# Performance work log

Measured on AMD Instinct MI355X. Metric: run time of the kernel, lower is better.

Reference implementation:

```python
import jax, jax.numpy as jnp
import numpy as np

B, T, S, H, D = 4, 2048, 2048, 16, 64


def setup_inputs() -> dict:
    key = jax.random.key(0)
    kq, kkv = jax.random.split(key)
    q = jax.random.normal(kq, (B, T, H, D), dtype=jnp.float32)
    kv = jax.random.normal(kkv, (B, S, 2, H, D), dtype=jnp.float32)
    return {"q": q, "kv": kv}


def reference(q, kv):
    # q: [B,T,H,D]; kv: [B,S,2,H,D] (packed k and v)
    k = kv[:, :, 0]  # [B,S,H,D]
    v = kv[:, :, 1]  # [B,S,H,D]
    scale = 1.0 / jnp.sqrt(jnp.asarray(q.shape[-1], q.dtype))
    # scores: [B,H,T,S]
    scores = jnp.einsum("bthd,bshd->bhts", q, k) * scale
    probs = jax.nn.softmax(scores, axis=-1)
    out = jnp.einsum("bhts,bshd->bthd", probs, v)  # [B,T,H,D]
    return out
```

## Files before the change

kernel.cpp:

```cpp
#include <hip/hip_runtime.h>
#include <hip/hip_bf16.h>

#define Bq 4
#define Tq 2048
#define Sq 2048
#define Hq 16
#define Dq 64
#define KVBLK 64
#define NT (Sq / KVBLK)

typedef short bf16x8 __attribute__((ext_vector_type(8)));
typedef short bf16x4 __attribute__((ext_vector_type(4)));
typedef float f32x4 __attribute__((ext_vector_type(4)));
typedef float f32x16 __attribute__((ext_vector_type(16)));
typedef int   i32x4 __attribute__((ext_vector_type(4)));
typedef int   i32x2 __attribute__((ext_vector_type(2)));
typedef unsigned int u32;

#if defined(__HIP_DEVICE_COMPILE__)
#if __has_builtin(__builtin_amdgcn_mfma_f32_32x32x16_bf16)
#define HAVE_MFMA32 1
#endif
#if __has_builtin(__builtin_amdgcn_mfma_f32_16x16x16bf16_1k)
#define HAVE_MFMA16 1
#endif
#if __has_builtin(__builtin_amdgcn_exp2f)
#define HAVE_EXP2 1
#endif
#endif
#ifndef HAVE_MFMA32
#define HAVE_MFMA32 0
#endif
#ifndef HAVE_MFMA16
#define HAVE_MFMA16 0
#endif
#ifndef HAVE_EXP2
#define HAVE_EXP2 0
#endif

static __device__ __forceinline__ f32x16 mfma32(bf16x8 a, bf16x8 b, f32x16 c) {
#if HAVE_MFMA32
    return __builtin_amdgcn_mfma_f32_32x32x16_bf16(a, b, c, 0, 0, 0);
#else
    return c;
#endif
}

static __device__ __forceinline__ f32x4 pv_mfma16(bf16x4 vf, bf16x4 pf, f32x4 acc) {
#if HAVE_MFMA16
    return __builtin_amdgcn_mfma_f32_16x16x16bf16_1k(vf, pf, acc, 0, 0, 0);
#else
    return acc;
#endif
}

static __device__ __forceinline__ float fexp2(float x) {
#if HAVE_EXP2
    return __builtin_amdgcn_exp2f(x);
#else
    return exp2f(x);
#endif
}

static __device__ __forceinline__ u32 pk2f(float a, float b) {
#if defined(__HIP_DEVICE_COMPILE__)
    __hip_bfloat162 h = __float22bfloat162_rn(make_float2(a, b));
    u32 r; __builtin_memcpy(&r, &h, 4);
    return r;
#else
    return 0u;
#endif
}

static __device__ __forceinline__ u32 pkc(float a, float b) {
    u32 ua = __float_as_uint(a); ua += 0x7fffu + ((ua >> 16) & 1u);
    u32 ub = __float_as_uint(b); ub += 0x7fffu + ((ub >> 16) & 1u);
    return (ua >> 16) | (ub & 0xffff0000u);
}

static __device__ __forceinline__ void gload16(const void* g, void* l) {
    __builtin_amdgcn_global_load_lds(
        (const __attribute__((address_space(1))) u32*)g,
        (__attribute__((address_space(3))) u32*)l, 16, 0, 0);
}

__global__ __launch_bounds__(256) void prepass(const float* __restrict__ kvp,
                                               char* __restrict__ wsK,
                                               char* __restrict__ wsV)
{
    if (blockIdx.x < 8192) {
        const int t = blockIdx.x * 256 + threadIdx.x;
        const int dq = t & 15, h = (t >> 4) & 15, s = (t >> 8) & 2047, b = t >> 19;
        const float* p = kvp + ((size_t)(b * 2048 + s)) * 2048 + h * 64 + dq * 4;
        const f32x4 f = *(const f32x4*)p;
        i32x2 w; w[0] = (int)pkc(f[0], f[1]); w[1] = (int)pkc(f[2], f[3]);
        const int r   = s & 63;
        const int pos = (r & 0x33) | (((r >> 2) & 1) << 3) | (((r >> 3) & 1) << 2);
        char* d = wsK + (size_t)(b * 16 + h) * 262144 + (s >> 6) * 8192
                + pos * 128 + ((dq * 8) ^ ((pos & 7) << 4));
        *(i32x2*)d = w;
    } else {
        const int t2 = (blockIdx.x - 8192) * 256 + threadIdx.x;
        const int dd = t2 & 63, h = (t2 >> 6) & 15, sq = (t2 >> 10) & 511, b = t2 >> 19;
        const float* p = kvp + ((size_t)(b * 2048 + sq * 4)) * 2048 + 1024 + h * 64 + dd;
        const float v0 = p[0], v1 = p[2048], v2 = p[4096], v3 = p[6144];
        i32x2 w; w[0] = (int)pkc(v0, v1); w[1] = (int)pkc(v2, v3);
        char* d = wsV + (size_t)(b * 16 + h) * 262144 + (sq >> 4) * 8192
                + dd * 128 + ((((sq & 15) * 8)) ^ ((dd & 7) << 4));
        *(i32x2*)d = w;
    }
}

__global__ __launch_bounds__(256, 2) void fattn_main(
    const float* __restrict__ q, const char* __restrict__ wsK,
    const char* __restrict__ wsV, float* __restrict__ out)
{
    __shared__ __align__(16) char Kl[2][8192];
    __shared__ __align__(16) char Vt[2][8192];

    const int tid  = threadIdx.x;
    const int lane = tid & 63;
    const int col  = lane & 31;
    const int hi   = lane >> 5;
    const int wid  = tid >> 6;

    const int lbid = ((blockIdx.x & 7) << 6) | (blockIdx.x >> 3);
    const int qt = lbid & 7;
    const int bh = lbid >> 3;
    const int b  = bh >> 4;
    const int h  = bh & 15;

    const float QSCL = 0.125f * 1.4426950408889634f;

    const int qrowA = (qt << 8) + (wid << 6) + col;
    const float* qpA = q + (((size_t)b * Tq + qrowA) * Hq + h) * Dq;
    const float* qpB = qpA + (size_t)32 * Hq * Dq;
    bf16x8 aqA[4], aqB[4];
#pragma unroll
    for (int k = 0; k < 4; ++k) {
        const int d0 = k * 16 + hi * 8;
        {
            f32x4 f0 = *(const f32x4*)(qpA + d0);
            f32x4 f1 = *(const f32x4*)(qpA + d0 + 4);
            i32x4 w;
            w[0] = (int)pk2f(f0[0] * QSCL, f0[1] * QSCL);
            w[1] = (int)pk2f(f0[2] * QSCL, f0[3] * QSCL);
            w[2] = (int)pk2f(f1[0] * QSCL, f1[1] * QSCL);
            w[3] = (int)pk2f(f1[2] * QSCL, f1[3] * QSCL);
            aqA[k] = __builtin_bit_cast(bf16x8, w);
        }
        {
            f32x4 f0 = *(const f32x4*)(qpB + d0);
            f32x4 f1 = *(const f32x4*)(qpB + d0 + 4);
            i32x4 w;
            w[0] = (int)pk2f(f0[0] * QSCL, f0[1] * QSCL);
            w[1] = (int)pk2f(f0[2] * QSCL, f0[3] * QSCL);
            w[2] = (int)pk2f(f1[0] * QSCL, f1[1] * QSCL);
            w[3] = (int)pk2f(f1[2] * QSCL, f1[3] * QSCL);
            aqB[k] = __builtin_bit_cast(bf16x8, w);
        }
    }

    const char* gK = wsK + (size_t)bh * 262144;
    const char* gV = wsV + (size_t)bh * 262144;
    const int go = tid * 16;

    auto STAGE = [&](int t) {
        const int bp = (t & 1) * 8192;
        const char* gk = gK + t * 8192;
        const char* gv = gV + t * 8192;
        char* lk = &Kl[0][0] + bp + wid * 1024;
        char* lv = &Vt[0][0] + bp + wid * 1024;
        gload16(gk + go, lk);
        gload16(gk + 4096 + go, lk + 4096);
        gload16(gv + go, lv);
        gload16(gv + 4096 + go, lv + 4096);
    };

    STAGE(0);

    f32x16 oA0{}, oA1{}, oB0{}, oB1{}, lA{}, lB{};
    const f32x16 z16{};
    const int kswz = (col & 7) << 4;
    const bf16x8 vones8 = {(short)0x3F80, (short)0x3F80, (short)0x3F80, (short)0x3F80,
                           (short)0x3F80, (short)0x3F80, (short)0x3F80, (short)0x3F80};

#pragma unroll 2
    for (int t = 0; t < NT; ++t) {
        __syncthreads();
        if (t + 1 < NT) STAGE(t + 1);
        const char* Kb = &Kl[0][0] + (t & 1) * 8192;
        const char* Vb = &Vt[0][0] + (t & 1) * 8192;

#pragma unroll
        for (int h2 = 0; h2 < 2; ++h2) {
            f32x16 sA, sB;
            __builtin_amdgcn_s_setprio(1);
            {
                const char* kr = Kb + (32 * h2 + col) * 128;
                bf16x8 kf = *(const bf16x8*)(kr + ((hi * 16) ^ kswz));
                sA = mfma32(kf, aqA[0], z16);
                sB = mfma32(kf, aqB[0], z16);
#pragma unroll
                for (int k = 1; k < 4; ++k) {
                    kf = *(const bf16x8*)(kr + ((k * 32 + hi * 16) ^ kswz));
                    sA = mfma32(kf, aqA[k], sA);
                    sB = mfma32(kf, aqB[k], sB);
                }
            }
            __builtin_amdgcn_s_setprio(0);

#pragma unroll
            for (int r = 0; r < 16; ++r) {
                sA[r] = fexp2(sA[r]);
                sB[r] = fexp2(sB[r]);
            }

            __builtin_amdgcn_s_setprio(1);
#pragma unroll
            for (int kp = 0; kp < 2; ++kp) {
                i32x4 wA, wB;
                wA[0] = (int)pk2f(sA[8 * kp + 0], sA[8 * kp + 1]);
                wA[1] = (int)pk2f(sA[8 * kp + 2], sA[8 * kp + 3]);
                wA[2] = (int)pk2f(sA[8 * kp + 4], sA[8 * kp + 5]);
                wA[3] = (int)pk2f(sA[8 * kp + 6], sA[8 * kp + 7]);
                wB[0] = (int)pk2f(sB[8 * kp + 0], sB[8 * kp + 1]);
                wB[1] = (int)pk2f(sB[8 * kp + 2], sB[8 * kp + 3]);
                wB[2] = (int)pk2f(sB[8 * kp + 4], sB[8 * kp + 5]);
                wB[3] = (int)pk2f(sB[8 * kp + 6], sB[8 * kp + 7]);
                const bf16x8 pfA = __builtin_bit_cast(bf16x8, wA);
                const bf16x8 pfB = __builtin_bit_cast(bf16x8, wB);
                const int voff = (64 * h2 + 32 * kp + 16 * hi) ^ kswz;
                bf16x8 vf0 = *(const bf16x8*)(Vb + col * 128 + voff);
                bf16x8 vf1 = *(const bf16x8*)(Vb + (32 + col) * 128 + voff);
                oA0 = mfma32(vf0, pfA, oA0);
                oA1 = mfma32(vf1, pfA, oA1);
                oB0 = mfma32(vf0, pfB, oB0);
                oB1 = mfma32(vf1, pfB, oB1);
                lA  = mfma32(vones8, pfA, lA);
                lB  = mfma32(vones8, pfB, lB);
            }
            __builtin_amdgcn_s_setprio(0);
        }
    }

    const float invA = 1.0f / lA[0];
    const float invB = 1.0f / lB[0];
    float* opA = out + (((size_t)b * Tq + qrowA) * Hq + h) * Dq;
    float* opB = opA + (size_t)32 * Hq * Dq;
#pragma unroll
    for (int mi = 0; mi < 4; ++mi) {
        f32x4 a0, a1, b0, b1;
#pragma unroll
        for (int j = 0; j < 4; ++j) {
            a0[j] = oA0[4*mi+j] * invA; a1[j] = oA1[4*mi+j] * invA;
            b0[j] = oB0[4*mi+j] * invB; b1[j] = oB1[4*mi+j] * invB;
        }
        *(f32x4*)(opA + mi * 8 + hi * 4)      = a0;
        *(f32x4*)(opA + 32 + mi * 8 + hi * 4) = a1;
        *(f32x4*)(opB + mi * 8 + hi * 4)      = b0;
        *(f32x4*)(opB + 32 + mi * 8 + hi * 4) = b1;
    }
}

__global__ __launch_bounds__(256, 4) void fattn_v4(
    const float* __restrict__ q, const float* __restrict__ kvp,
    float* __restrict__ out)
{
    __shared__ __align__(16) short Kl[2][KVBLK * 64];
    __shared__ __align__(16) short Vt[2][64 * KVBLK];

    const int tid = threadIdx.x;
    const int c   = tid & 15;
    const int g   = (tid >> 4) & 3;
    const int wid = tid >> 6;

    const int lbid = ((blockIdx.x & 7) << 8) | (blockIdx.x >> 3);
    const int qt = lbid & 31;
    const int bh = lbid >> 5;
    const int b  = bh >> 4;
    const int h  = bh & 15;

    const float QSCL = 0.125f * 1.4426950408889634f;

    const int qrow = (qt << 6) + (wid << 4) + c;
    const float* qp = q + (((size_t)b * Tq + qrow) * Hq + h) * Dq;
    bf16x8 aq[2];
#pragma unroll
    for (int kc = 0; kc < 2; ++kc) {
        f32x4 f0 = *(const f32x4*)(qp + kc * 32 + g * 8);
        f32x4 f1 = *(const f32x4*)(qp + kc * 32 + g * 8 + 4);
        i32x4 w;
        w[0] = (int)pkc(f0[0] * QSCL, f0[1] * QSCL);
        w[1] = (int)pkc(f0[2] * QSCL, f0[3] * QSCL);
        w[2] = (int)pkc(f1[0] * QSCL, f1[1] * QSCL);
        w[3] = (int)pkc(f1[2] * QSCL, f1[3] * QSCL);
        aq[kc] = __builtin_bit_cast(bf16x8, w);
    }

    const int ksr = tid >> 2;
    const int ksd = (tid & 3) << 4;
    const int vw4 = tid >> 4;
    const int vd0 = (tid & 15) << 2;

    const float* kbase = kvp + (size_t)b * Sq * 2 * Hq * Dq + h * Dq;
    f32x4 kr0, kr1, kr2, kr3, vr0, vr1, vr2, vr3;

    auto ISSUE = [&](int t) {
        const float* kp = kbase + (size_t)(t * KVBLK + ksr) * 2048 + ksd;
        kr0 = *(const f32x4*)(kp);
        kr1 = *(const f32x4*)(kp + 4);
        kr2 = *(const f32x4*)(kp + 8);
        kr3 = *(const f32x4*)(kp + 12);
        const float* vp = kbase + (size_t)(t * KVBLK + (vw4 << 2)) * 2048 + 1024 + vd0;
        vr0 = *(const f32x4*)(vp);
        vr1 = *(const f32x4*)(vp + 2048);
        vr2 = *(const f32x4*)(vp + 4096);
        vr3 = *(const f32x4*)(vp + 6144);
    };
    auto WRITE = [&](int t) {
        const int bp = t & 1;
        char* Kb = (char*)Kl[bp];
        char* Vb = (char*)Vt[bp];
        const int kswz = (ksr & 7) << 4;
        i32x4 w;
        w[0] = (int)pkc(kr0[0], kr0[1]); w[1] = (int)pkc(kr0[2], kr0[3]);
        w[2] = (int)pkc(kr1[0], kr1[1]); w[3] = (int)pkc(kr1[2], kr1[3]);
        *(bf16x8*)(Kb + ksr * 128 + (((ksd << 1)     ) ^ kswz)) = __builtin_bit_cast(bf16x8, w);
        w[0] = (int)pkc(kr2[0], kr2[1]); w[1] = (int)pkc(kr2[2], kr2[3]);
        w[2] = (int)pkc(kr3[0], kr3[1]); w[3] = (int)pkc(kr3[2], kr3[3]);
        *(bf16x8*)(Kb + ksr * 128 + (((ksd << 1) + 16) ^ kswz)) = __builtin_bit_cast(bf16x8, w);
#pragma unroll
        for (int j = 0; j < 4; ++j) {
            i32x2 t2;
            t2[0] = (int)pkc(vr0[j], vr1[j]);
            t2[1] = (int)pkc(vr2[j], vr3[j]);
            const int row = vd0 + j;
            *(i32x2*)(Vb + row * 128 + ((vw4 << 3) ^ ((row & 7) << 4))) = t2;
        }
    };

    ISSUE(0);
    WRITE(0);

    float m_r = -1e30f, l_r = 0.f;
    f32x4 oacc[4];
#pragma unroll
    for (int dt = 0; dt < 4; ++dt) oacc[dt] = (f32x4){0.f, 0.f, 0.f, 0.f};
    const int cswz = (c & 7) << 4;

    for (int t = 0; t < NT; ++t) {
        __syncthreads();
        const char* Kb = (const char*)Kl[t & 1];
        const char* Vb = (const char*)Vt[t & 1];

        f32x4 sac[4];
#pragma unroll
        for (int ks = 0; ks < 4; ++ks) {
            const char* rb = Kb + ((ks << 4) + c) * 128;
            bf16x8 kf0 = *(const bf16x8*)(rb + (((g << 4)     ) ^ cswz));
            bf16x8 kf1 = *(const bf16x8*)(rb + ((64 + (g << 4)) ^ cswz));
            f32x4 z = (f32x4){0.f, 0.f, 0.f, 0.f};
            z = __builtin_amdgcn_mfma_f32_16x16x32_bf16(kf0, aq[0], z, 0, 0, 0);
            z = __builtin_amdgcn_mfma_f32_16x16x32_bf16(kf1, aq[1], z, 0, 0, 0);
            sac[ks] = z;
        }
        ISSUE(t + 1 < NT ? t + 1 : NT - 1);

        float vmax = sac[0][0];
#pragma unroll
        for (int ks = 0; ks < 4; ++ks)
#pragma unroll
            for (int r = 0; r < 4; ++r) vmax = fmaxf(vmax, sac[ks][r]);
        vmax = fmaxf(vmax, __shfl_xor(vmax, 16, 64));
        vmax = fmaxf(vmax, __shfl_xor(vmax, 32, 64));
        if (__any(vmax > m_r + 10.0f)) {
            const float mnew  = fmaxf(m_r, vmax);
            const float alpha = exp2f(m_r - mnew);
            m_r = mnew;
            l_r *= alpha;
#pragma unroll
            for (int dt = 0; dt < 4; ++dt) oacc[dt] *= alpha;
        }
        float ssum = 0.f;
#pragma unroll
        for (int ks = 0; ks < 4; ++ks)
#pragma unroll
            for (int r = 0; r < 4; ++r) {
                const float p = exp2f(sac[ks][r] - m_r);
                sac[ks][r] = p;
                ssum += p;
            }
        ssum += __shfl_xor(ssum, 16, 64);
        ssum += __shfl_xor(ssum, 32, 64);
        l_r += ssum;

#pragma unroll
        for (int ks = 0; ks < 4; ++ks) {
            i32x2 pp;
            pp[0] = (int)pkc(sac[ks][0], sac[ks][1]);
            pp[1] = (int)pkc(sac[ks][2], sac[ks][3]);
            const bf16x4 pf = __builtin_bit_cast(bf16x4, pp);
#pragma unroll
            for (int dt = 0; dt < 4; ++dt) {
                const i32x2 vv = *(const i32x2*)(Vb + ((dt << 4) + c) * 128 +
                                   (((ks << 5) + (g << 3)) ^ cswz));
                const bf16x4 vf = __builtin_bit_cast(bf16x4, vv);
                oacc[dt] = pv_mfma16(vf, pf, oacc[dt]);
            }
        }
        WRITE(t + 1);
    }

    const float inv = 1.0f / l_r;
    float* op = out + (((size_t)b * Tq + qrow) * Hq + h) * Dq;
#pragma unroll
    for (int dt = 0; dt < 4; ++dt) {
        f32x4 o = oacc[dt] * inv;
        *(f32x4*)(op + (dt << 4) + (g << 2)) = o;
    }
}

extern "C" void kernel_launch(void* const* d_in, const int* in_sizes, int n_in,
                              void* d_out, int out_size, void* d_ws, size_t ws_size,
                              hipStream_t stream) {
    const float* q  = (const float*)d_in[0];
    const float* kv = (const float*)d_in[1];
    float* out = (float*)d_out;
    if (ws_size >= (size_t)33554432) {
        char* wsK = (char*)d_ws;
        char* wsV = wsK + 16777216;
        prepass<<<dim3(16384), dim3(256), 0, stream>>>(kv, wsK, wsV);
        fattn_main<<<dim3(512), dim3(256), 0, stream>>>(q, wsK, wsV, out);
    } else {
        fattn_v4<<<dim3(2048), dim3(256), 0, stream>>>(q, kv, out);
    }
}
```

Baseline: 106.4 us.

## Load pre-fragmented K/V tiles directly to registers, drop LDS staging

The prepass now writes K and V into a per-lane MFMA fragment order, so the main kernel loads each tile straight from global memory into registers with coalesced 16-byte loads. This removes the shared-memory double buffer and the per-tile __syncthreads, and the two register buffers are ping-ponged so the next tile is prefetched while the current one is computed. The row-sum MFMAs against a ones vector are replaced by scalar sums plus a cross-half shuffle, which cuts matrix-unit work. In exchange, 32 extra bf16x8 registers per thread raise register pressure and may lower occupancy, and each wave now reads K/V from global or L2 on its own instead of sharing one LDS copy per block.

```diff
diff --git a/kernel.cpp b/kernel.cpp
--- a/kernel.cpp
+++ b/kernel.cpp
@@ -78,46 +78,53 @@
     return (ua >> 16) | (ub & 0xffff0000u);
 }
 
-static __device__ __forceinline__ void gload16(const void* g, void* l) {
-    __builtin_amdgcn_global_load_lds(
-        (const __attribute__((address_space(1))) u32*)g,
-        (__attribute__((address_space(3))) u32*)l, 16, 0, 0);
+static __device__ __forceinline__ float sum16(const f32x16& s) {
+    float a0 = s[0]+s[1],  a1 = s[2]+s[3],  a2 = s[4]+s[5],   a3 = s[6]+s[7];
+    float a4 = s[8]+s[9],  a5 = s[10]+s[11], a6 = s[12]+s[13], a7 = s[14]+s[15];
+    float b0 = a0+a1, b1 = a2+a3, b2 = a4+a5, b3 = a6+a7;
+    return (b0+b1)+(b2+b3);
 }
 
 __global__ __launch_bounds__(256) void prepass(const float* __restrict__ kvp,
-                                               char* __restrict__ wsK,
-                                               char* __restrict__ wsV)
+                                               char* __restrict__ ws)
 {
-    if (blockIdx.x < 8192) {
-        const int t = blockIdx.x * 256 + threadIdx.x;
-        const int dq = t & 15, h = (t >> 4) & 15, s = (t >> 8) & 2047, b = t >> 19;
-        const float* p = kvp + ((size_t)(b * 2048 + s)) * 2048 + h * 64 + dq * 4;
-        const f32x4 f = *(const f32x4*)p;
-        i32x2 w; w[0] = (int)pkc(f[0], f[1]); w[1] = (int)pkc(f[2], f[3]);
-        const int r   = s & 63;
-        const int pos = (r & 0x33) | (((r >> 2) & 1) << 3) | (((r >> 3) & 1) << 2);
-        char* d = wsK + (size_t)(b * 16 + h) * 262144 + (s >> 6) * 8192
-                + pos * 128 + ((dq * 8) ^ ((pos & 7) << 4));
-        *(i32x2*)d = w;
+    const int gid  = blockIdx.x * 256 + threadIdx.x;
+    const int half = gid >> 20;
+    const int g    = gid & 0xFFFFF;
+    const int l    = g & 63;
+    const int f    = (g >> 6) & 7;
+    const int tile = (g >> 9) & 31;
+    const int bh   = (g >> 14) & 63;
+    const int b = bh >> 4, h = bh & 15;
+    char* dst = ws + (size_t)bh * 524288 + (size_t)tile * 16384
+              + (half ? (8 + f) : f) * 1024 + l * 16;
+    i32x4 w;
+    if (half == 0) {
+        const int h2 = f >> 2, k = f & 3, hi = l >> 5, c32 = l & 31;
+        const int r  = 32 * h2 + ((c32 & 0x33) | (((c32 >> 2) & 1) << 3) | (((c32 >> 3) & 1) << 2));
+        const int d0 = 16 * k + 8 * hi;
+        const float* p = kvp + ((size_t)(b * 2048 + tile * 64 + r)) * 2048 + h * 64 + d0;
+        const f32x4 a = *(const f32x4*)p;
+        const f32x4 c = *(const f32x4*)(p + 4);
+        w[0] = (int)pkc(a[0], a[1]); w[1] = (int)pkc(a[2], a[3]);
+        w[2] = (int)pkc(c[0], c[1]); w[3] = (int)pkc(c[2], c[3]);
     } else {
-        const int t2 = (blockIdx.x - 8192) * 256 + threadIdx.x;
-        const int dd = t2 & 63, h = (t2 >> 6) & 15, sq = (t2 >> 10) & 511, b = t2 >> 19;
-        const float* p = kvp + ((size_t)(b * 2048 + sq * 4)) * 2048 + 1024 + h * 64 + dd;
-        const float v0 = p[0], v1 = p[2048], v2 = p[4096], v3 = p[6144];
-        i32x2 w; w[0] = (int)pkc(v0, v1); w[1] = (int)pkc(v2, v3);
-        char* d = wsV + (size_t)(b * 16 + h) * 262144 + (sq >> 4) * 8192
-                + dd * 128 + ((((sq & 15) * 8)) ^ ((dd & 7) << 4));
-        *(i32x2*)d = w;
-    }
+        const int h2 = f >> 2, kp = (f >> 1) & 1, vh = f & 1, hi = l >> 5, col = l & 31;
+        const int d   = 32 * vh + col;
+        const int kv0 = 32 * h2 + 16 * kp + 8 * hi;
+        const float* p = kvp + ((size_t)(b * 2048 + tile * 64 + kv0)) * 2048 + 1024 + h * 64 + d;
+        w[0] = (int)pkc(p[0],         p[2048]);
+        w[1] = (int)pkc(p[2 * 2048],  p[3 * 2048]);
+        w[2] = (int)pkc(p[4 * 2048],  p[5 * 2048]);
+        w[3] = (int)pkc(p[6 * 2048],  p[7 * 2048]);
+    }
+    *(i32x4*)dst = w;
 }
 
 __global__ __launch_bounds__(256, 2) void fattn_main(
-    const float* __restrict__ q, const char* __restrict__ wsK,
-    const char* __restrict__ wsV, float* __restrict__ out)
+    const float* __restrict__ q, const char* __restrict__ ws,
+    float* __restrict__ out)
 {
-    __shared__ __align__(16) char Kl[2][8192];
-    __shared__ __align__(16) char Vt[2][8192];
-
     const int tid  = threadIdx.x;
     const int lane = tid & 63;
     const int col  = lane & 31;
@@ -161,52 +168,34 @@
         }
     }
 
-    const char* gK = wsK + (size_t)bh * 262144;
-    const char* gV = wsV + (size_t)bh * 262144;
-    const int go = tid * 16;
-
-    auto STAGE = [&](int t) {
-        const int bp = (t & 1) * 8192;
-        const char* gk = gK + t * 8192;
-        const char* gv = gV + t * 8192;
-        char* lk = &Kl[0][0] + bp + wid * 1024;
-        char* lv = &Vt[0][0] + bp + wid * 1024;
-        gload16(gk + go, lk);
-        gload16(gk + 4096 + go, lk + 4096);
-        gload16(gv + go, lv);
-        gload16(gv + 4096 + go, lv + 4096);
+    const char* gw = ws + (size_t)bh * 524288 + lane * 16;
+
+    bf16x8 fA[16], fB[16];
+    auto STAGE = [&](bf16x8* F, int t) {
+        const char* gt = gw + (size_t)t * 16384;
+#pragma unroll
+        for (int f = 0; f < 16; ++f)
+            F[f] = *(const bf16x8*)(gt + f * 1024);
     };
 
-    STAGE(0);
-
-    f32x16 oA0{}, oA1{}, oB0{}, oB1{}, lA{}, lB{};
+    f32x16 oA0{}, oA1{}, oB0{}, oB1{};
+    float lrA = 0.f, lrB = 0.f;
     const f32x16 z16{};
-    const int kswz = (col & 7) << 4;
-    const bf16x8 vones8 = {(short)0x3F80, (short)0x3F80, (short)0x3F80, (short)0x3F80,
-                           (short)0x3F80, (short)0x3F80, (short)0x3F80, (short)0x3F80};
-
-#pragma unroll 2
-    for (int t = 0; t < NT; ++t) {
-        __syncthreads();
-        if (t + 1 < NT) STAGE(t + 1);
-        const char* Kb = &Kl[0][0] + (t & 1) * 8192;
-        const char* Vb = &Vt[0][0] + (t & 1) * 8192;
-
+
+    STAGE(fA, 0);
+    STAGE(fB, 1);
+
+    auto COMPUTE = [&](const bf16x8* F) {
 #pragma unroll
         for (int h2 = 0; h2 < 2; ++h2) {
             f32x16 sA, sB;
             __builtin_amdgcn_s_setprio(1);
-            {
-                const char* kr = Kb + (32 * h2 + col) * 128;
-                bf16x8 kf = *(const bf16x8*)(kr + ((hi * 16) ^ kswz));
-                sA = mfma32(kf, aqA[0], z16);
-                sB = mfma32(kf, aqB[0], z16);
-#pragma unroll
-                for (int k = 1; k < 4; ++k) {
-                    kf = *(const bf16x8*)(kr + ((k * 32 + hi * 16) ^ kswz));
-                    sA = mfma32(kf, aqA[k], sA);
-                    sB = mfma32(kf, aqB[k], sB);
-                }
+            sA = mfma32(F[h2 * 4 + 0], aqA[0], z16);
+            sB = mfma32(F[h2 * 4 + 0], aqB[0], z16);
+#pragma unroll
+            for (int k = 1; k < 4; ++k) {
+                sA = mfma32(F[h2 * 4 + k], aqA[k], sA);
+                sB = mfma32(F[h2 * 4 + k], aqB[k], sB);
             }
             __builtin_amdgcn_s_setprio(0);
 
@@ -215,6 +204,8 @@
                 sA[r] = fexp2(sA[r]);
                 sB[r] = fexp2(sB[r]);
             }
+            lrA += sum16(sA);
+            lrB += sum16(sB);
 
             __builtin_amdgcn_s_setprio(1);
 #pragma unroll
@@ -230,22 +221,28 @@
                 wB[3] = (int)pk2f(sB[8 * kp + 6], sB[8 * kp + 7]);
                 const bf16x8 pfA = __builtin_bit_cast(bf16x8, wA);
                 const bf16x8 pfB = __builtin_bit_cast(bf16x8, wB);
-                const int voff = (64 * h2 + 32 * kp + 16 * hi) ^ kswz;
-                bf16x8 vf0 = *(const bf16x8*)(Vb + col * 128 + voff);
-                bf16x8 vf1 = *(const bf16x8*)(Vb + (32 + col) * 128 + voff);
+                const bf16x8 vf0 = F[8 + (h2 * 2 + kp) * 2 + 0];
+                const bf16x8 vf1 = F[8 + (h2 * 2 + kp) * 2 + 1];
                 oA0 = mfma32(vf0, pfA, oA0);
                 oA1 = mfma32(vf1, pfA, oA1);
                 oB0 = mfma32(vf0, pfB, oB0);
                 oB1 = mfma32(vf1, pfB, oB1);
-                lA  = mfma32(vones8, pfA, lA);
-                lB  = mfma32(vones8, pfB, lB);
             }
             __builtin_amdgcn_s_setprio(0);
         }
-    }
-
-    const float invA = 1.0f / lA[0];
-    const float invB = 1.0f / lB[0];
+    };
+
+    for (int tt = 0; tt < NT / 2; ++tt) {
+        COMPUTE(fA);
+        if (2 * tt + 2 < NT) STAGE(fA, 2 * tt + 2);
+        COMPUTE(fB);
+        if (2 * tt + 3 < NT) STAGE(fB, 2 * tt + 3);
+    }
+
+    const float lAf = lrA + __shfl_xor(lrA, 32, 64);
+    const float lBf = lrB + __shfl_xor(lrB, 32, 64);
+    const float invA = 1.0f / lAf;
+    const float invB = 1.0f / lBf;
     float* opA = out + (((size_t)b * Tq + qrowA) * Hq + h) * Dq;
     float* opB = opA + (size_t)32 * Hq * Dq;
 #pragma unroll
@@ -253,8 +250,8 @@
         f32x4 a0, a1, b0, b1;
 #pragma unroll
         for (int j = 0; j < 4; ++j) {
-            a0[j] = oA0[4*mi+j] * invA; a1[j] = oA1[4*mi+j] * invA;
-            b0[j] = oB0[4*mi+j] * invB; b1[j] = oB1[4*mi+j] * invB;
+            a0[j] = oA0[4 * mi + j] * invA; a1[j] = oA1[4 * mi + j] * invA;
+            b0[j] = oB0[4 * mi + j] * invB; b1[j] = oB1[4 * mi + j] * invB;
         }
         *(f32x4*)(opA + mi * 8 + hi * 4)      = a0;
         *(f32x4*)(opA + 32 + mi * 8 + hi * 4) = a1;
@@ -428,10 +425,9 @@
     const float* kv = (const float*)d_in[1];
     float* out = (float*)d_out;
     if (ws_size >= (size_t)33554432) {
-        char* wsK = (char*)d_ws;
-        char* wsV = wsK + 16777216;
-        prepass<<<dim3(16384), dim3(256), 0, stream>>>(kv, wsK, wsV);
-        fattn_main<<<dim3(512), dim3(256), 0, stream>>>(q, wsK, wsV, out);
+        char* ws = (char*)d_ws;
+        prepass<<<dim3(8192), dim3(256), 0, stream>>>(kv, ws);
+        fattn_main<<<dim3(512), dim3(256), 0, stream>>>(q, ws, out);
     } else {
         fattn_v4<<<dim3(2048), dim3(256), 0, stream>>>(q, kv, out);
     }
```

Result: slower. 349.3 us (+228.5%).

## Stage two KV tiles per barrier and compute row sums with VALU adds

Applied to the files above, without the earlier changes.

The main attention loop now loads two 64-row KV tiles per stage into a four-slot LDS ring and processes both between barriers, which halves the number of __syncthreads. The row-sum accumulation that used extra MFMAs against a ones vector is replaced by per-lane scalar sums of the exp values, combined across half-waves with a shuffle at the end. This removes two MFMAs per inner step but adds VALU adds. LDS usage doubles to 32 KB per block, which may limit occupancy at two blocks per CU. The row sum now comes from the unrounded fp32 exp values while the PV product uses bf16-rounded ones, which slightly changes normalization.

```diff
diff --git a/kernel.cpp b/kernel.cpp
--- a/kernel.cpp
+++ b/kernel.cpp
@@ -82,6 +82,13 @@
     __builtin_amdgcn_global_load_lds(
         (const __attribute__((address_space(1))) u32*)g,
         (__attribute__((address_space(3))) u32*)l, 16, 0, 0);
+}
+
+static __device__ __forceinline__ float sum16(const f32x16& s) {
+    float a0 = s[0]+s[1],  a1 = s[2]+s[3],  a2 = s[4]+s[5],   a3 = s[6]+s[7];
+    float a4 = s[8]+s[9],  a5 = s[10]+s[11], a6 = s[12]+s[13], a7 = s[14]+s[15];
+    float b0 = a0+a1, b1 = a2+a3, b2 = a4+a5, b3 = a6+a7;
+    return (b0+b1)+(b2+b3);
 }
 
 __global__ __launch_bounds__(256) void prepass(const float* __restrict__ kvp,
@@ -115,8 +122,8 @@
     const float* __restrict__ q, const char* __restrict__ wsK,
     const char* __restrict__ wsV, float* __restrict__ out)
 {
-    __shared__ __align__(16) char Kl[2][8192];
-    __shared__ __align__(16) char Vt[2][8192];
+    __shared__ __align__(16) char Kl[2][2][8192];
+    __shared__ __align__(16) char Vt[2][2][8192];
 
     const int tid  = threadIdx.x;
     const int lane = tid & 63;
@@ -165,33 +172,28 @@
     const char* gV = wsV + (size_t)bh * 262144;
     const int go = tid * 16;
 
-    auto STAGE = [&](int t) {
-        const int bp = (t & 1) * 8192;
+    auto STAGE = [&](int t, int slot) {
         const char* gk = gK + t * 8192;
         const char* gv = gV + t * 8192;
-        char* lk = &Kl[0][0] + bp + wid * 1024;
-        char* lv = &Vt[0][0] + bp + wid * 1024;
+        char* lk = &Kl[0][0][0] + slot * 8192 + wid * 1024;
+        char* lv = &Vt[0][0][0] + slot * 8192 + wid * 1024;
         gload16(gk + go, lk);
         gload16(gk + 4096 + go, lk + 4096);
         gload16(gv + go, lv);
         gload16(gv + 4096 + go, lv + 4096);
     };
 
-    STAGE(0);
-
-    f32x16 oA0{}, oA1{}, oB0{}, oB1{}, lA{}, lB{};
+    STAGE(0, 0);
+    STAGE(1, 1);
+
+    f32x16 oA0{}, oA1{}, oB0{}, oB1{};
+    float lrA = 0.f, lrB = 0.f;
     const f32x16 z16{};
     const int kswz = (col & 7) << 4;
-    const bf16x8 vones8 = {(short)0x3F80, (short)0x3F80, (short)0x3F80, (short)0x3F80,
-                           (short)0x3F80, (short)0x3F80, (short)0x3F80, (short)0x3F80};
-
-#pragma unroll 2
-    for (int t = 0; t < NT; ++t) {
-        __syncthreads();
-        if (t + 1 < NT) STAGE(t + 1);
-        const char* Kb = &Kl[0][0] + (t & 1) * 8192;
-        const char* Vb = &Vt[0][0] + (t & 1) * 8192;
-
+
+    auto COMPUTE = [&](int slot) {
+        const char* Kb = &Kl[0][0][0] + slot * 8192;
+        const char* Vb = &Vt[0][0][0] + slot * 8192;
 #pragma unroll
         for (int h2 = 0; h2 < 2; ++h2) {
             f32x16 sA, sB;
@@ -215,6 +217,8 @@
                 sA[r] = fexp2(sA[r]);
                 sB[r] = fexp2(sB[r]);
             }
+            lrA += sum16(sA);
+            lrB += sum16(sB);
 
             __builtin_amdgcn_s_setprio(1);
 #pragma unroll
@@ -237,15 +241,27 @@
                 oA1 = mfma32(vf1, pfA, oA1);
                 oB0 = mfma32(vf0, pfB, oB0);
                 oB1 = mfma32(vf1, pfB, oB1);
-                lA  = mfma32(vones8, pfA, lA);
-                lB  = mfma32(vones8, pfB, lB);
             }
             __builtin_amdgcn_s_setprio(0);
         }
-    }
-
-    const float invA = 1.0f / lA[0];
-    const float invB = 1.0f / lB[0];
+    };
+
+    const int NW = NT / 2;
+    for (int w = 0; w < NW; ++w) {
+        __syncthreads();
+        const int buf = w & 1;
+        if (w + 1 < NW) {
+            STAGE(2 * w + 2, (buf ^ 1) * 2 + 0);
+            STAGE(2 * w + 3, (buf ^ 1) * 2 + 1);
+        }
+        COMPUTE(buf * 2 + 0);
+        COMPUTE(buf * 2 + 1);
+    }
+
+    const float lAf = lrA + __shfl_xor(lrA, 32, 64);
+    const float lBf = lrB + __shfl_xor(lrB, 32, 64);
+    const float invA = 1.0f / lAf;
+    const float invB = 1.0f / lBf;
     float* opA = out + (((size_t)b * Tq + qrowA) * Hq + h) * Dq;
     float* opB = opA + (size_t)32 * Hq * Dq;
 #pragma unroll
@@ -253,8 +269,8 @@
         f32x4 a0, a1, b0, b1;
 #pragma unroll
         for (int j = 0; j < 4; ++j) {
-            a0[j] = oA0[4*mi+j] * invA; a1[j] = oA1[4*mi+j] * invA;
-            b0[j] = oB0[4*mi+j] * invB; b1[j] = oB1[4*mi+j] * invB;
+            a0[j] = oA0[4 * mi + j] * invA; a1[j] = oA1[4 * mi + j] * invA;
+            b0[j] = oB0[4 * mi + j] * invB; b1[j] = oB1[4 * mi + j] * invB;
         }
         *(f32x4*)(opA + mi * 8 + hi * 4)      = a0;
         *(f32x4*)(opA + 32 + mi * 8 + hi * 4) = a1;
```

Measured after the change: 102.8 us, median of 2. 3.3% less time.
